# Performance work log

Hardware: AMD Instinct MI355X
Metric: run time of the kernel (lower is better)

## Reference

```python
import jax, jax.numpy as jnp
import numpy as np

N_IN = 25000     # source points
N_OUT = 25000    # query points
K = 32           # neighbors per query point
D_COORD = 3
D_FEAT = 64
D_HID = 128
D_OUT = 64


def setup_inputs() -> dict:
    key = jax.random.key(0)
    ks = jax.random.split(key, 8)
    y = jax.random.normal(ks[0], (N_IN, D_COORD), dtype=jnp.float32)
    x = jax.random.normal(ks[1], (N_OUT, D_COORD), dtype=jnp.float32)
    f_y = jax.random.normal(ks[2], (N_IN, D_FEAT), dtype=jnp.float32)
    d_in = 2 * D_COORD + D_FEAT  # 70
    W1 = jax.random.normal(ks[3], (d_in, D_HID), dtype=jnp.float32) / np.sqrt(d_in)
    b1 = jnp.zeros((D_HID,), dtype=jnp.float32)
    W2 = jax.random.normal(ks[4], (D_HID, D_OUT), dtype=jnp.float32) / np.sqrt(D_HID)
    b2 = jnp.zeros((D_OUT,), dtype=jnp.float32)
    a = jax.random.normal(ks[5], (D_HID,), dtype=jnp.float32) / np.sqrt(D_HID)
    neighbors_index = jax.random.randint(ks[6], (N_OUT * K,), 0, N_IN, dtype=jnp.int64)
    return {"y": y, "x": x, "f_y": f_y, "W1": W1, "b1": b1,
            "W2": W2, "b2": b2, "a": a, "neighbors_index": neighbors_index}


def reference(y, x, f_y, W1, b1, W2, b2, a, neighbors_index):
    E = neighbors_index.shape[0]           # N_OUT * K edges
    n_out = E // K
    # --- irregular gather of neighbor coords + features ---
    y_g = y[neighbors_index]               # [E, 3]
    f_g = f_y[neighbors_index]             # [E, 64]
    x_rep = jnp.repeat(x, K, axis=0)       # [E, 3]
    edge_in = jnp.concatenate([y_g, x_rep, f_g], axis=-1)  # [E, 70]
    # --- per-edge channel MLP ---
    h = jax.nn.gelu(edge_in @ W1 + b1)     # [E, 128]
    m = h @ W2 + b2                        # [E, 64]
    # --- attention weights, softmax within each neighborhood of K ---
    scores = (h @ a).reshape(n_out, K)     # [n_out, K]
    alpha = jax.nn.softmax(scores, axis=-1)
    # --- weighted scatter-reduce (regular K-block form) ---
    out = jnp.einsum('nk,nkd->nd', alpha, m.reshape(n_out, K, D_OUT))
    return out                             # [n_out, 64]
```

## Files before the change

### kernel.cpp

```cpp
#include <hip/hip_runtime.h>

typedef __attribute__((ext_vector_type(8)))  short bf16x8;
typedef __attribute__((ext_vector_type(16))) float f32x16;
typedef __attribute__((ext_vector_type(2)))  float f32x2;

#define KNBR 32
#define WAVES 8

union Frag { int4 i; bf16x8 b; };

__device__ __forceinline__ unsigned short f2bf(float f) {
    unsigned u = __float_as_uint(f);
    u += 0x7FFFu + ((u >> 16) & 1u);
    return (unsigned short)(u >> 16);
}

__device__ __forceinline__ unsigned cvt_pk_bf16(float lo, float hi) {
    unsigned r;
    asm("v_cvt_pk_bf16_f32 %0, %1, %2" : "=v"(r) : "v"(lo), "v"(hi));
    return r;
}

__device__ __forceinline__ f32x2 fast_gelu2(f32x2 v) {
    const f32x2 c1v  = {0.044715f, 0.044715f};
    const f32x2 onev = {1.0f, 1.0f};
    const f32x2 K2v  = {-2.3022081951f, -2.3022081951f};
    f32x2 p = v * __builtin_elementwise_fma(c1v, v * v, onev);
    f32x2 t = K2v * p;
    float e0, e1, r0, r1;
    asm("v_exp_f32 %0, %1" : "=v"(e0) : "v"(t.x));
    asm("v_exp_f32 %0, %1" : "=v"(e1) : "v"(t.y));
    f32x2 ev = {e0, e1};
    f32x2 d = ev + onev;
    asm("v_rcp_f32 %0, %1" : "=v"(r0) : "v"(d.x));
    asm("v_rcp_f32 %0, %1" : "=v"(r1) : "v"(d.y));
    f32x2 rv = {r0, r1};
    return v * rv;
}

__global__ __launch_bounds__(256) void conv_fy_kernel(
    const float* __restrict__ f_y, int4* __restrict__ fyb, int n8)
{
    const int i = blockIdx.x * 256 + threadIdx.x;
    if (i < n8) {
        const float4* s = (const float4*)(f_y + (long)i * 8);
        float4 v0 = s[0], v1 = s[1];
        int4 p;
        p.x = cvt_pk_bf16(v0.x, v0.y);
        p.y = cvt_pk_bf16(v0.z, v0.w);
        p.z = cvt_pk_bf16(v1.x, v1.y);
        p.w = cvt_pk_bf16(v1.z, v1.w);
        fyb[i] = p;
    }
}

__global__ __launch_bounds__(256) void pack_weights_kernel(
    const float* __restrict__ W1, const float* __restrict__ W2,
    const float* __restrict__ b1, const float* __restrict__ av,
    int4* __restrict__ W1p, int4* __restrict__ W2p, float* __restrict__ avp)
{
    const int idx = blockIdx.x * 256 + threadIdx.x;
    unsigned short vals[8];
    if (idx < 1280) {
        const int a = idx >> 6, l = idx & 63;
        const int Mt = a / 5, ks = a - Mt * 5;
        const int row = Mt * 32 + (l & 31), hi = l >> 5;
        #pragma unroll
        for (int e = 0; e < 8; ++e) {
            const int slot = ks * 16 + hi * 8 + e;
            float f;
            if      (slot < 64)  f = W1[(slot + 6) * 128 + row];
            else if (slot < 70)  f = W1[(slot - 64) * 128 + row];
            else if (slot == 70) f = b1[row];
            else                 f = 0.0f;
            vals[e] = f2bf(f);
        }
        int4 v;
        v.x = vals[0] | (vals[1] << 16); v.y = vals[2] | (vals[3] << 16);
        v.z = vals[4] | (vals[5] << 16); v.w = vals[6] | (vals[7] << 16);
        W1p[idx] = v;
    } else if (idx < 2304) {
        const int i2 = idx - 1280;
        const int rgn = i2 >> 6, l = i2 & 63;
        const int Nt = rgn >> 3, ks2 = rgn & 7;
        const int col = Nt * 32 + (l & 31), hi = l >> 5;
        #pragma unroll
        for (int e = 0; e < 8; ++e) {
            const int Mt = ks2 >> 1;
            const int t  = 2 * (ks2 & 1) + (e >> 2);
            const int c  = e & 3;
            const int hid = Mt * 32 + 4 * (2 * t + hi) + c;
            vals[e] = f2bf(W2[hid * 64 + col]);
        }
        int4 v;
        v.x = vals[0] | (vals[1] << 16); v.y = vals[2] | (vals[3] << 16);
        v.z = vals[4] | (vals[5] << 16); v.w = vals[6] | (vals[7] << 16);
        W2p[i2] = v;
    } else if (idx < 2432) {
        const int r_ = idx - 2304;
        const int Mt = r_ >> 5, hi = (r_ >> 4) & 1, r = r_ & 15;
        avp[r_] = av[Mt * 32 + 8 * (r >> 2) + 4 * hi + (r & 3)];
    }
}

__global__ __launch_bounds__(512, 4) void it_mfma_kernel(
    const float* __restrict__ y,
    const float* __restrict__ xq,
    const int4*  __restrict__ fyb,
    const float* __restrict__ b2,
    const int*   __restrict__ nbr,
    const int4*  __restrict__ Wall,
    float*       __restrict__ out,
    int n_out)
{
    __shared__ int4  sW[2304];
    __shared__ float sAv[128];

    const int tid = threadIdx.x;
    const int w   = tid >> 6;
    const int l   = tid & 63;
    const int el  = l & 31;
    const int hi  = l >> 5;

    const int q = blockIdx.x * WAVES + w;
    const bool active = (q < n_out);
    const int qc = active ? q : 0;

    const int ni = nbr[qc * KNBR + el];

    #pragma unroll
    for (int t = 0; t < 5; ++t) {
        const int idx = tid + t * 512;
        if (idx < 2304) sW[idx] = Wall[idx];
    }
    if (tid < 128) sAv[tid] = ((const float*)(Wall + 2304))[tid];

    const int4* fb = fyb + (long)ni * 8;
    Frag B1[5];
    B1[0].i = fb[0 + hi];
    B1[1].i = fb[2 + hi];
    B1[2].i = fb[4 + hi];
    B1[3].i = fb[6 + hi];
    float2 y01 = {0.f, 0.f}, x01 = {0.f, 0.f};
    float  yz = 0.f, xz = 0.f;
    if (hi == 0) {
        y01 = *(const float2*)(y + ni * 3);
        yz  = y[ni * 3 + 2];
        x01 = *(const float2*)(xq + qc * 3);
        xz  = xq[qc * 3 + 2];
    }
    __syncthreads();
    const int4* sW1 = sW;
    const int4* sW2 = sW + 1280;

    if (!active) return;

    B1[4].i = make_int4(0, 0, 0, 0);
    if (hi == 0) {
        B1[4].i.x = cvt_pk_bf16(y01.x, y01.y);
        B1[4].i.y = cvt_pk_bf16(yz,    x01.x);
        B1[4].i.z = cvt_pk_bf16(x01.y, xz);
        B1[4].i.w = cvt_pk_bf16(1.0f,  0.0f);
    }

    const f32x16 z16 = {0.f,0.f,0.f,0.f,0.f,0.f,0.f,0.f,
                        0.f,0.f,0.f,0.f,0.f,0.f,0.f,0.f};

    Frag A2[8];
    f32x2 scv = {0.f, 0.f};
    #pragma unroll
    for (int p = 0; p < 2; ++p) {
        f32x16 aA = z16, aB = z16;
        #pragma unroll
        for (int ks = 0; ks < 5; ++ks) {
            Frag wa0, wa1;
            wa0.i = sW1[((2 * p + 0) * 5 + ks) * 64 + l];
            wa1.i = sW1[((2 * p + 1) * 5 + ks) * 64 + l];
            aA = __builtin_amdgcn_mfma_f32_32x32x16_bf16(wa0.b, B1[ks].b, aA, 0, 0, 0);
            aB = __builtin_amdgcn_mfma_f32_32x32x16_bf16(wa1.b, B1[ks].b, aB, 0, 0, 0);
        }
        #pragma unroll
        for (int m = 0; m < 2; ++m) {
            const f32x16 ac = m ? aB : aA;
            const int Mt = 2 * p + m;
            const float* avb = sAv + Mt * 32 + hi * 16;
            float4 av0 = *(const float4*)(avb + 0);
            float4 av1 = *(const float4*)(avb + 4);
            float4 av2 = *(const float4*)(avb + 8);
            float4 av3 = *(const float4*)(avb + 12);
            f32x2 avv[8] = {{av0.x, av0.y}, {av0.z, av0.w},
                            {av1.x, av1.y}, {av1.z, av1.w},
                            {av2.x, av2.y}, {av2.z, av2.w},
                            {av3.x, av3.y}, {av3.z, av3.w}};
            unsigned hw[8];
            #pragma unroll
            for (int i = 0; i < 8; ++i) {
                f32x2 vin = {ac[2 * i], ac[2 * i + 1]};
                f32x2 hv = fast_gelu2(vin);
                scv = __builtin_elementwise_fma(hv, avv[i], scv);
                hw[i] = cvt_pk_bf16(hv.x, hv.y);
            }
            A2[2 * Mt + 0].i.x = hw[0];
            A2[2 * Mt + 0].i.y = hw[1];
            A2[2 * Mt + 0].i.z = hw[2];
            A2[2 * Mt + 0].i.w = hw[3];
            A2[2 * Mt + 1].i.x = hw[4];
            A2[2 * Mt + 1].i.y = hw[5];
            A2[2 * Mt + 1].i.z = hw[6];
            A2[2 * Mt + 1].i.w = hw[7];
        }
    }

    Frag wf[8];
    #pragma unroll
    for (int ks2 = 0; ks2 < 8; ++ks2)
        wf[ks2].i = sW2[(0 * 8 + ks2) * 64 + l];

    float sc = scv.x + scv.y;
    sc += __shfl_xor(sc, 32, 64);
    float mx = sc;
    mx = fmaxf(mx, __shfl_xor(mx, 1, 64));
    mx = fmaxf(mx, __shfl_xor(mx, 2, 64));
    mx = fmaxf(mx, __shfl_xor(mx, 4, 64));
    mx = fmaxf(mx, __shfl_xor(mx, 8, 64));
    mx = fmaxf(mx, __shfl_xor(mx, 16, 64));
    float ex = __expf(sc - mx);
    float sm = ex;
    sm += __shfl_xor(sm, 1, 64);
    sm += __shfl_xor(sm, 2, 64);
    sm += __shfl_xor(sm, 4, 64);
    sm += __shfl_xor(sm, 8, 64);
    sm += __shfl_xor(sm, 16, 64);
    const float alpha = __fdividef(ex, sm);

    f32x16 o0 = z16, o1 = z16;
    #pragma unroll
    for (int ks2 = 0; ks2 < 8; ++ks2) {
        Frag w1;
        w1.i = sW2[(1 * 8 + ks2) * 64 + l];
        o0 = __builtin_amdgcn_mfma_f32_32x32x16_bf16(A2[ks2].b, wf[ks2].b, o0, 0, 0, 0);
        o1 = __builtin_amdgcn_mfma_f32_32x32x16_bf16(A2[ks2].b, w1.b, o1, 0, 0, 0);
    }

    float ar[16];
    #pragma unroll
    for (int r = 0; r < 16; ++r)
        ar[r] = __shfl(alpha, 8 * (r >> 2) + 4 * hi + (r & 3), 64);

    #pragma unroll
    for (int nt = 0; nt < 2; ++nt) {
        const f32x16 oo = nt ? o1 : o0;
        f32x2 acc = {0.f, 0.f};
        #pragma unroll
        for (int i = 0; i < 8; ++i) {
            f32x2 ov = {oo[2 * i], oo[2 * i + 1]};
            f32x2 av2 = {ar[2 * i], ar[2 * i + 1]};
            acc = __builtin_elementwise_fma(ov, av2, acc);
        }
        float o = acc.x + acc.y;
        o += __shfl_xor(o, 32, 64);
        if (l < 32)
            out[qc * 64 + nt * 32 + l] = o + b2[nt * 32 + l];
    }
}

extern "C" void kernel_launch(void* const* d_in, const int* in_sizes, int n_in,
                              void* d_out, int out_size, void* d_ws, size_t ws_size,
                              hipStream_t stream) {
    const float* y   = (const float*)d_in[0];
    const float* xq  = (const float*)d_in[1];
    const float* f_y = (const float*)d_in[2];
    const float* W1  = (const float*)d_in[3];
    const float* b1  = (const float*)d_in[4];
    const float* W2  = (const float*)d_in[5];
    const float* b2  = (const float*)d_in[6];
    const float* av  = (const float*)d_in[7];
    const int*   nbr = (const int*)d_in[8];
    float* out = (float*)d_out;

    const int n_out = in_sizes[1] / 3;
    const int nfy   = in_sizes[2];

    int4*  W1p = (int4*)d_ws;
    int4*  W2p = W1p + 1280;
    float* avp = (float*)(W1p + 2304);
    int4*  fyb = W1p + 2336;

    pack_weights_kernel<<<10, 256, 0, stream>>>(W1, W2, b1, av, W1p, W2p, avp);
    const int n8 = nfy / 8;
    conv_fy_kernel<<<(n8 + 255) / 256, 256, 0, stream>>>(f_y, fyb, n8);
    const int nblk = (n_out + WAVES - 1) / WAVES;
    it_mfma_kernel<<<nblk, 512, 0, stream>>>(y, xq, fyb, b2, nbr,
                                             W1p, out, n_out);
}
```

Baseline: 70.66 us.

## Use persistent grid with prefetch of next query's gather; merge prep kernels

The main kernel becomes persistent, with at most 1024 blocks whose waves loop over queries with a grid stride. Each iteration software-prefetches the next query's neighbor indices, bf16 features and coordinates, overlapping gather latency with the MFMA work. Weight staging into LDS now happens once per block instead of once per eight queries. The two preprocessing kernels are fused into one launch. The costs are higher register pressure from the prefetch buffers and fewer resident blocks, which could hurt latency hiding.

Result: slower. 76.30 us (+8.0%).

```diff
diff --git a/kernel.cpp b/kernel.cpp
--- a/kernel.cpp
+++ b/kernel.cpp
@@ -38,26 +38,12 @@
     return v * rv;
 }
 
-__global__ __launch_bounds__(256) void conv_fy_kernel(
-    const float* __restrict__ f_y, int4* __restrict__ fyb, int n8)
-{
-    const int i = blockIdx.x * 256 + threadIdx.x;
-    if (i < n8) {
-        const float4* s = (const float4*)(f_y + (long)i * 8);
-        float4 v0 = s[0], v1 = s[1];
-        int4 p;
-        p.x = cvt_pk_bf16(v0.x, v0.y);
-        p.y = cvt_pk_bf16(v0.z, v0.w);
-        p.z = cvt_pk_bf16(v1.x, v1.y);
-        p.w = cvt_pk_bf16(v1.z, v1.w);
-        fyb[i] = p;
-    }
-}
-
-__global__ __launch_bounds__(256) void pack_weights_kernel(
+__global__ __launch_bounds__(256) void prep_kernel(
     const float* __restrict__ W1, const float* __restrict__ W2,
     const float* __restrict__ b1, const float* __restrict__ av,
-    int4* __restrict__ W1p, int4* __restrict__ W2p, float* __restrict__ avp)
+    const float* __restrict__ f_y,
+    int4* __restrict__ W1p, int4* __restrict__ W2p, float* __restrict__ avp,
+    int4* __restrict__ fyb, int n8)
 {
     const int idx = blockIdx.x * 256 + threadIdx.x;
     unsigned short vals[8];
@@ -100,6 +86,18 @@
         const int r_ = idx - 2304;
         const int Mt = r_ >> 5, hi = (r_ >> 4) & 1, r = r_ & 15;
         avp[r_] = av[Mt * 32 + 8 * (r >> 2) + 4 * hi + (r & 3)];
+    } else {
+        const int i = idx - 2432;
+        if (i < n8) {
+            const float4* s = (const float4*)(f_y + (long)i * 8);
+            float4 v0 = s[0], v1 = s[1];
+            int4 p;
+            p.x = cvt_pk_bf16(v0.x, v0.y);
+            p.y = cvt_pk_bf16(v0.z, v0.w);
+            p.z = cvt_pk_bf16(v1.x, v1.y);
+            p.w = cvt_pk_bf16(v1.z, v1.w);
+            fyb[i] = p;
+        }
     }
 }
 
@@ -111,7 +109,7 @@
     const int*   __restrict__ nbr,
     const int4*  __restrict__ Wall,
     float*       __restrict__ out,
-    int n_out)
+    int n_out, int nwaves)
 {
     __shared__ int4  sW[2304];
     __shared__ float sAv[128];
@@ -121,12 +119,6 @@
     const int l   = tid & 63;
     const int el  = l & 31;
     const int hi  = l >> 5;
-
-    const int q = blockIdx.x * WAVES + w;
-    const bool active = (q < n_out);
-    const int qc = active ? q : 0;
-
-    const int ni = nbr[qc * KNBR + el];
 
     #pragma unroll
     for (int t = 0; t < 5; ++t) {
@@ -135,132 +127,152 @@
     }
     if (tid < 128) sAv[tid] = ((const float*)(Wall + 2304))[tid];
 
-    const int4* fb = fyb + (long)ni * 8;
-    Frag B1[5];
-    B1[0].i = fb[0 + hi];
-    B1[1].i = fb[2 + hi];
-    B1[2].i = fb[4 + hi];
-    B1[3].i = fb[6 + hi];
-    float2 y01 = {0.f, 0.f}, x01 = {0.f, 0.f};
-    float  yz = 0.f, xz = 0.f;
+    int q = blockIdx.x * WAVES + w;
+    const int q0c = (q < n_out) ? q : 0;
+
+    int ni = nbr[q0c * KNBR + el];
+    const int4* fp0 = fyb + (long)ni * 8;
+    int4 st0 = fp0[0 + hi], st1 = fp0[2 + hi];
+    int4 st2 = fp0[4 + hi], st3 = fp0[6 + hi];
+    float2 sy01 = {0.f, 0.f}, sx01 = {0.f, 0.f};
+    float  syz = 0.f, sxz = 0.f;
     if (hi == 0) {
-        y01 = *(const float2*)(y + ni * 3);
-        yz  = y[ni * 3 + 2];
-        x01 = *(const float2*)(xq + qc * 3);
-        xz  = xq[qc * 3 + 2];
+        sy01 = *(const float2*)(y + ni * 3);
+        syz  = y[ni * 3 + 2];
+        sx01 = *(const float2*)(xq + q0c * 3);
+        sxz  = xq[q0c * 3 + 2];
     }
+    int qn = q + nwaves;
+    int ni_next = nbr[((qn < n_out) ? qn : q0c) * KNBR + el];
+
     __syncthreads();
     const int4* sW1 = sW;
     const int4* sW2 = sW + 1280;
 
-    if (!active) return;
-
-    B1[4].i = make_int4(0, 0, 0, 0);
-    if (hi == 0) {
-        B1[4].i.x = cvt_pk_bf16(y01.x, y01.y);
-        B1[4].i.y = cvt_pk_bf16(yz,    x01.x);
-        B1[4].i.z = cvt_pk_bf16(x01.y, xz);
-        B1[4].i.w = cvt_pk_bf16(1.0f,  0.0f);
-    }
+    if (q >= n_out) return;
 
     const f32x16 z16 = {0.f,0.f,0.f,0.f,0.f,0.f,0.f,0.f,
                         0.f,0.f,0.f,0.f,0.f,0.f,0.f,0.f};
 
-    Frag A2[8];
-    f32x2 scv = {0.f, 0.f};
-    #pragma unroll
-    for (int p = 0; p < 2; ++p) {
-        f32x16 aA = z16, aB = z16;
-        #pragma unroll
-        for (int ks = 0; ks < 5; ++ks) {
-            Frag wa0, wa1;
-            wa0.i = sW1[((2 * p + 0) * 5 + ks) * 64 + l];
-            wa1.i = sW1[((2 * p + 1) * 5 + ks) * 64 + l];
-            aA = __builtin_amdgcn_mfma_f32_32x32x16_bf16(wa0.b, B1[ks].b, aA, 0, 0, 0);
-            aB = __builtin_amdgcn_mfma_f32_32x32x16_bf16(wa1.b, B1[ks].b, aB, 0, 0, 0);
-        }
-        #pragma unroll
-        for (int m = 0; m < 2; ++m) {
-            const f32x16 ac = m ? aB : aA;
-            const int Mt = 2 * p + m;
-            const float* avb = sAv + Mt * 32 + hi * 16;
-            float4 av0 = *(const float4*)(avb + 0);
-            float4 av1 = *(const float4*)(avb + 4);
-            float4 av2 = *(const float4*)(avb + 8);
-            float4 av3 = *(const float4*)(avb + 12);
-            f32x2 avv[8] = {{av0.x, av0.y}, {av0.z, av0.w},
-                            {av1.x, av1.y}, {av1.z, av1.w},
-                            {av2.x, av2.y}, {av2.z, av2.w},
-                            {av3.x, av3.y}, {av3.z, av3.w}};
-            unsigned hw[8];
+    for (; q < n_out; q += nwaves) {
+        Frag B1[5];
+        B1[0].i = st0; B1[1].i = st1; B1[2].i = st2; B1[3].i = st3;
+        B1[4].i = make_int4(0, 0, 0, 0);
+        if (hi == 0) {
+            B1[4].i.x = cvt_pk_bf16(sy01.x, sy01.y);
+            B1[4].i.y = cvt_pk_bf16(syz,    sx01.x);
+            B1[4].i.z = cvt_pk_bf16(sx01.y, sxz);
+            B1[4].i.w = cvt_pk_bf16(1.0f,   0.0f);
+        }
+
+        const int qnext = q + nwaves;
+        {
+            const int4* fn = fyb + (long)ni_next * 8;
+            st0 = fn[0 + hi]; st1 = fn[2 + hi];
+            st2 = fn[4 + hi]; st3 = fn[6 + hi];
+            if (hi == 0) {
+                sy01 = *(const float2*)(y + ni_next * 3);
+                syz  = y[ni_next * 3 + 2];
+                const int qx = (qnext < n_out) ? qnext : q;
+                sx01 = *(const float2*)(xq + qx * 3);
+                sxz  = xq[qx * 3 + 2];
+            }
+            const int qnn = qnext + nwaves;
+            ni_next = nbr[((qnn < n_out) ? qnn : q) * KNBR + el];
+        }
+
+        Frag A2[8];
+        f32x2 scv = {0.f, 0.f};
+        #pragma unroll
+        for (int p = 0; p < 2; ++p) {
+            f32x16 aA = z16, aB = z16;
+            #pragma unroll
+            for (int ks = 0; ks < 5; ++ks) {
+                Frag wa0, wa1;
+                wa0.i = sW1[((2 * p + 0) * 5 + ks) * 64 + l];
+                wa1.i = sW1[((2 * p + 1) * 5 + ks) * 64 + l];
+                aA = __builtin_amdgcn_mfma_f32_32x32x16_bf16(wa0.b, B1[ks].b, aA, 0, 0, 0);
+                aB = __builtin_amdgcn_mfma_f32_32x32x16_bf16(wa1.b, B1[ks].b, aB, 0, 0, 0);
+            }
+            #pragma unroll
+            for (int m = 0; m < 2; ++m) {
+                const f32x16 ac = m ? aB : aA;
+                const int Mt = 2 * p + m;
+                const float* avb = sAv + Mt * 32 + hi * 16;
+                float4 av0 = *(const float4*)(avb + 0);
+                float4 av1 = *(const float4*)(avb + 4);
+                float4 av2 = *(const float4*)(avb + 8);
+                float4 av3 = *(const float4*)(avb + 12);
+                f32x2 avv[8] = {{av0.x, av0.y}, {av0.z, av0.w},
+                                {av1.x, av1.y}, {av1.z, av1.w},
+                                {av2.x, av2.y}, {av2.z, av2.w},
+                                {av3.x, av3.y}, {av3.z, av3.w}};
+                unsigned hw[8];
+                #pragma unroll
+                for (int i = 0; i < 8; ++i) {
+                    f32x2 vin = {ac[2 * i], ac[2 * i + 1]};
+                    f32x2 hv = fast_gelu2(vin);
+                    scv = __builtin_elementwise_fma(hv, avv[i], scv);
+                    hw[i] = cvt_pk_bf16(hv.x, hv.y);
+                }
+                A2[2 * Mt + 0].i.x = hw[0];
+                A2[2 * Mt + 0].i.y = hw[1];
+                A2[2 * Mt + 0].i.z = hw[2];
+                A2[2 * Mt + 0].i.w = hw[3];
+                A2[2 * Mt + 1].i.x = hw[4];
+                A2[2 * Mt + 1].i.y = hw[5];
+                A2[2 * Mt + 1].i.z = hw[6];
+                A2[2 * Mt + 1].i.w = hw[7];
+            }
+        }
+
+        float sc = scv.x + scv.y;
+        sc += __shfl_xor(sc, 32, 64);
+        float mx = sc;
+        mx = fmaxf(mx, __shfl_xor(mx, 1, 64));
+        mx = fmaxf(mx, __shfl_xor(mx, 2, 64));
+        mx = fmaxf(mx, __shfl_xor(mx, 4, 64));
+        mx = fmaxf(mx, __shfl_xor(mx, 8, 64));
+        mx = fmaxf(mx, __shfl_xor(mx, 16, 64));
+        float ex = __expf(sc - mx);
+        float sm = ex;
+        sm += __shfl_xor(sm, 1, 64);
+        sm += __shfl_xor(sm, 2, 64);
+        sm += __shfl_xor(sm, 4, 64);
+        sm += __shfl_xor(sm, 8, 64);
+        sm += __shfl_xor(sm, 16, 64);
+        const float alpha = __fdividef(ex, sm);
+
+        f32x16 o0 = z16, o1 = z16;
+        #pragma unroll
+        for (int ks2 = 0; ks2 < 8; ++ks2) {
+            Frag w0, w1;
+            w0.i = sW2[(0 * 8 + ks2) * 64 + l];
+            w1.i = sW2[(1 * 8 + ks2) * 64 + l];
+            o0 = __builtin_amdgcn_mfma_f32_32x32x16_bf16(A2[ks2].b, w0.b, o0, 0, 0, 0);
+            o1 = __builtin_amdgcn_mfma_f32_32x32x16_bf16(A2[ks2].b, w1.b, o1, 0, 0, 0);
+        }
+
+        float ar[16];
+        #pragma unroll
+        for (int r = 0; r < 16; ++r)
+            ar[r] = __shfl(alpha, 8 * (r >> 2) + 4 * hi + (r & 3), 64);
+
+        #pragma unroll
+        for (int nt = 0; nt < 2; ++nt) {
+            const f32x16 oo = nt ? o1 : o0;
+            f32x2 acc = {0.f, 0.f};
             #pragma unroll
             for (int i = 0; i < 8; ++i) {
-                f32x2 vin = {ac[2 * i], ac[2 * i + 1]};
-                f32x2 hv = fast_gelu2(vin);
-                scv = __builtin_elementwise_fma(hv, avv[i], scv);
-                hw[i] = cvt_pk_bf16(hv.x, hv.y);
+                f32x2 ov = {oo[2 * i], oo[2 * i + 1]};
+                f32x2 av2 = {ar[2 * i], ar[2 * i + 1]};
+                acc = __builtin_elementwise_fma(ov, av2, acc);
             }
-            A2[2 * Mt + 0].i.x = hw[0];
-            A2[2 * Mt + 0].i.y = hw[1];
-            A2[2 * Mt + 0].i.z = hw[2];
-            A2[2 * Mt + 0].i.w = hw[3];
-            A2[2 * Mt + 1].i.x = hw[4];
-            A2[2 * Mt + 1].i.y = hw[5];
-            A2[2 * Mt + 1].i.z = hw[6];
-            A2[2 * Mt + 1].i.w = hw[7];
-        }
-    }
-
-    Frag wf[8];
-    #pragma unroll
-    for (int ks2 = 0; ks2 < 8; ++ks2)
-        wf[ks2].i = sW2[(0 * 8 + ks2) * 64 + l];
-
-    float sc = scv.x + scv.y;
-    sc += __shfl_xor(sc, 32, 64);
-    float mx = sc;
-    mx = fmaxf(mx, __shfl_xor(mx, 1, 64));
-    mx = fmaxf(mx, __shfl_xor(mx, 2, 64));
-    mx = fmaxf(mx, __shfl_xor(mx, 4, 64));
-    mx = fmaxf(mx, __shfl_xor(mx, 8, 64));
-    mx = fmaxf(mx, __shfl_xor(mx, 16, 64));
-    float ex = __expf(sc - mx);
-    float sm = ex;
-    sm += __shfl_xor(sm, 1, 64);
-    sm += __shfl_xor(sm, 2, 64);
-    sm += __shfl_xor(sm, 4, 64);
-    sm += __shfl_xor(sm, 8, 64);
-    sm += __shfl_xor(sm, 16, 64);
-    const float alpha = __fdividef(ex, sm);
-
-    f32x16 o0 = z16, o1 = z16;
-    #pragma unroll
-    for (int ks2 = 0; ks2 < 8; ++ks2) {
-        Frag w1;
-        w1.i = sW2[(1 * 8 + ks2) * 64 + l];
-        o0 = __builtin_amdgcn_mfma_f32_32x32x16_bf16(A2[ks2].b, wf[ks2].b, o0, 0, 0, 0);
-        o1 = __builtin_amdgcn_mfma_f32_32x32x16_bf16(A2[ks2].b, w1.b, o1, 0, 0, 0);
-    }
-
-    float ar[16];
-    #pragma unroll
-    for (int r = 0; r < 16; ++r)
-        ar[r] = __shfl(alpha, 8 * (r >> 2) + 4 * hi + (r & 3), 64);
-
-    #pragma unroll
-    for (int nt = 0; nt < 2; ++nt) {
-        const f32x16 oo = nt ? o1 : o0;
-        f32x2 acc = {0.f, 0.f};
-        #pragma unroll
-        for (int i = 0; i < 8; ++i) {
-            f32x2 ov = {oo[2 * i], oo[2 * i + 1]};
-            f32x2 av2 = {ar[2 * i], ar[2 * i + 1]};
-            acc = __builtin_elementwise_fma(ov, av2, acc);
-        }
-        float o = acc.x + acc.y;
-        o += __shfl_xor(o, 32, 64);
-        if (l < 32)
-            out[qc * 64 + nt * 32 + l] = o + b2[nt * 32 + l];
+            float o = acc.x + acc.y;
+            o += __shfl_xor(o, 32, 64);
+            if (l < 32)
+                out[q * 64 + nt * 32 + l] = o + b2[nt * 32 + l];
+        }
     }
 }
 
@@ -286,10 +298,14 @@
     float* avp = (float*)(W1p + 2304);
     int4*  fyb = W1p + 2336;
 
-    pack_weights_kernel<<<10, 256, 0, stream>>>(W1, W2, b1, av, W1p, W2p, avp);
     const int n8 = nfy / 8;
-    conv_fy_kernel<<<(n8 + 255) / 256, 256, 0, stream>>>(f_y, fyb, n8);
-    const int nblk = (n_out + WAVES - 1) / WAVES;
+    const int prep_blk = (2432 + n8 + 255) / 256;
+    prep_kernel<<<prep_blk, 256, 0, stream>>>(W1, W2, b1, av, f_y,
+                                              W1p, W2p, avp, fyb, n8);
+
+    int nblk = (n_out + WAVES - 1) / WAVES;
+    if (nblk > 1024) nblk = 1024;
+    const int nwaves = nblk * WAVES;
     it_mfma_kernel<<<nblk, 512, 0, stream>>>(y, xq, fyb, b2, nbr,
-                                             W1p, out, n_out);
-}
+                                             W1p, out, n_out, nwaves);
+}
```
